# Optimization experiments

Hardware: AMD Instinct MI355X
Metric: run time of the kernel (lower is better)

## Reference

```python
import jax, jax.numpy as jnp
import numpy as np

B = 4096   # batch
V = 512    # num_variables
H = 64     # hidden_dim


def setup_inputs() -> dict:
    key = jax.random.key(0)
    ks = jax.random.split(key, 6)
    return {
        "X": jax.random.normal(ks[0], (B, V), dtype=jnp.float32),
        "adjacency_logits": jax.random.normal(ks[1], (V, V), dtype=jnp.float32) * 0.1,
        # W1[i] is the first Linear of net i: maps V inputs -> H hidden
        "W1": jax.random.normal(ks[2], (V, V, H), dtype=jnp.float32) * (1.0 / np.sqrt(V)),
        "b1": jax.random.normal(ks[3], (V, H), dtype=jnp.float32) * 0.01,
        # W2[i] is the second Linear of net i: maps H hidden -> 1 output
        "W2": jax.random.normal(ks[4], (V, H), dtype=jnp.float32) * (1.0 / np.sqrt(H)),
        "b2": jax.random.normal(ks[5], (V,), dtype=jnp.float32) * 0.01,
    }


def reference(X, adjacency_logits, W1, b1, W2, b2):
    # Hard adjacency (hard_adjacency=True path): threshold sigmoid, zero diagonal.
    probs = jax.nn.sigmoid(adjacency_logits)
    adj = (probs > 0.5).astype(X.dtype) * (1.0 - jnp.eye(V, dtype=X.dtype))  # [V, V]

    # Original loop: for each i, net_i(X * adj[:, i]).
    # Fold the parent mask into the first-layer weights: W1_eff[i, v, h] = W1[i, v, h] * adj[v, i]
    W1_eff = W1 * adj.T[:, :, None]                      # [V, V, H]
    h = jax.nn.relu(jnp.einsum('bv,ivh->bih', X, W1_eff) + b1[None])  # [B, V, H]
    reconstructed = jnp.einsum('bih,ih->bi', h, W2) + b2[None]        # [B, V]
    return reconstructed, adj
```

## Files before the change

kernel.cpp:

```cpp
#include <hip/hip_runtime.h>
#include <hip/hip_bf16.h>
#include <stdint.h>

#define BB 4096
#define VV 512
#define HH 64

typedef short bf16x8 __attribute__((ext_vector_type(8)));
typedef float floatx4 __attribute__((ext_vector_type(4)));
typedef unsigned short ushort8 __attribute__((ext_vector_type(8)));

typedef const __attribute__((address_space(1))) void g_void;
typedef __attribute__((address_space(3))) void l_void;

__device__ __forceinline__ void gload_lds16(const void* g, void* l) {
    __builtin_amdgcn_global_load_lds((g_void*)g, (l_void*)l, 16, 0, 0);
}

__device__ __forceinline__ unsigned short f2bf_rne(float f) {
    unsigned int u = __float_as_uint(f);
    u += 0x7FFFu + ((u >> 16) & 1u);
    return (unsigned short)(u >> 16);
}

__global__ __launch_bounds__(256) void adj_kernel(const float* __restrict__ logits,
                                                  float* __restrict__ adj_out) {
    int idx = blockIdx.x * 256 + threadIdx.x;
    int v = idx >> 9, u = idx & (VV - 1);
    adj_out[idx] = (logits[idx] > 0.0f && v != u) ? 1.0f : 0.0f;
}

__global__ __launch_bounds__(256) void prep_kernel(const float* __restrict__ X,
                                                   const float* __restrict__ logits,
                                                   float* __restrict__ adj_out,
                                                   unsigned short* __restrict__ Xp) {
    int idx = blockIdx.x * 256 + threadIdx.x;
    {
        int v = idx >> 9, u = idx & (VV - 1);
        adj_out[idx] = (logits[idx] > 0.0f && v != u) ? 1.0f : 0.0f;
    }
    {
        int lane = idx & 63;
        int mt   = (idx >> 6) & 3;
        int ks   = (idx >> 8) & 15;
        int rb   = idx >> 12;
        int row  = rb * 64 + mt * 16 + (lane & 15);
        int k0   = ks * 32 + (lane >> 4) * 8;
        const float* src = X + (size_t)row * VV + k0;
        ushort8 o;
        #pragma unroll
        for (int e = 0; e < 8; ++e) o[e] = f2bf_rne(src[e]);
        *(ushort8*)(Xp + (size_t)idx * 8) = o;
    }
}

__global__ __launch_bounds__(256) void w1_transform_kernel(const float* __restrict__ W1,
                                                           const float* __restrict__ logits,
                                                           unsigned short* __restrict__ W1t) {
    __shared__ float tile[64][65];
    __shared__ float maskv[64];
    int bx = blockIdx.x;
    int i  = bx >> 3;
    int v0 = (bx & 7) << 6;
    int t  = threadIdx.x;
    if (t < 64) {
        int v = v0 + t;
        maskv[t] = (logits[(size_t)v * VV + i] > 0.0f && v != i) ? 1.0f : 0.0f;
    }
    const float* src = W1 + ((size_t)i * VV + v0) * HH;
    #pragma unroll
    for (int j = 0; j < 16; ++j) {
        int idx = j * 256 + t;
        tile[idx >> 6][idx & 63] = src[idx];
    }
    __syncthreads();
    unsigned short* dst = W1t + (size_t)i * (HH * VV) + v0;
    #pragma unroll
    for (int j = 0; j < 2; ++j) {
        int c = j * 256 + t;
        int h = c >> 3;
        int vr0 = (c & 7) * 8;
        ushort8 o;
        #pragma unroll
        for (int r = 0; r < 8; ++r)
            o[r] = f2bf_rne(tile[vr0 + r][h] * maskv[vr0 + r]);
        *(ushort8*)&dst[(size_t)h * VV + vr0] = o;
    }
}

__global__ __launch_bounds__(256, 2) void dag_gemm_kernel(
        const unsigned short* __restrict__ Xp,
        const unsigned short* __restrict__ W1t,
        const float* __restrict__ b1,
        const float* __restrict__ W2,
        const float* __restrict__ b2,
        float* __restrict__ outT)
{
    __shared__ __align__(16) unsigned short Ws[HH * VV];
    __shared__ float Po[256];

    const int t    = threadIdx.x;
    const int wave = t >> 6;
    const int lane = t & 63;
    const int ln   = lane & 15;
    const int quad = lane >> 4;

    const int bx   = blockIdx.x;
    const int i    = bx >> 4;
    const int row0 = (bx & 15) << 8;

    const unsigned short* abase =
        Xp + (size_t)((row0 >> 6) + wave) * (64 * VV) + lane * 8;

    bf16x8 af[4][4];
    #pragma unroll
    for (int s = 0; s < 3; ++s)
        #pragma unroll
        for (int mt = 0; mt < 4; ++mt)
            af[s][mt] = *(const bf16x8*)(abase + (s * 4 + mt) * 512);

    const unsigned short* wbase = W1t + (size_t)i * (HH * VV);
    #pragma unroll
    for (int j = 0; j < 16; ++j) {
        int c = j * 256 + t;
        int h = c >> 6, s = c & 63;
        gload_lds16(wbase + (size_t)h * VV + (size_t)(s ^ (h & 7)) * 8,
                    (char*)Ws + c * 16);
    }
    __syncthreads();

    floatx4 acc[4][4];
    #pragma unroll
    for (int a = 0; a < 4; ++a)
        #pragma unroll
        for (int b = 0; b < 4; ++b)
            acc[a][b] = (floatx4){0.f, 0.f, 0.f, 0.f};

    bf16x8 bq[2][4];
    #pragma unroll
    for (int nt = 0; nt < 4; ++nt)
        bq[0][nt] = *(const bf16x8*)&Ws[(nt * 16 + ln) * VV + (quad ^ (ln & 7)) * 8];

    #pragma unroll
    for (int kk = 0; kk < 16; ++kk) {
        const int cur = kk & 1, nxt = cur ^ 1;
        if (kk < 13) {
            #pragma unroll
            for (int mt = 0; mt < 4; ++mt)
                af[(kk + 3) & 3][mt] =
                    *(const bf16x8*)(abase + ((kk + 3) * 4 + mt) * 512);
        }
        if (kk < 15) {
            #pragma unroll
            for (int nt = 0; nt < 4; ++nt)
                bq[nxt][nt] = *(const bf16x8*)
                    &Ws[(nt * 16 + ln) * VV + (((kk + 1) * 4 + quad) ^ (ln & 7)) * 8];
        }
        #pragma unroll
        for (int mt = 0; mt < 4; ++mt)
            #pragma unroll
            for (int nt = 0; nt < 4; ++nt)
                acc[mt][nt] = __builtin_amdgcn_mfma_f32_16x16x32_bf16(
                    af[kk & 3][mt], bq[cur][nt], acc[mt][nt], 0, 0, 0);
    }

    float b1v[4], w2v[4];
    #pragma unroll
    for (int nt = 0; nt < 4; ++nt) {
        b1v[nt] = b1[i * HH + nt * 16 + ln];
        w2v[nt] = W2[i * HH + nt * 16 + ln];
    }
    const float b2i = b2[i];
    #pragma unroll
    for (int mt = 0; mt < 4; ++mt) {
        #pragma unroll
        for (int r = 0; r < 4; ++r) {
            float p = 0.f;
            #pragma unroll
            for (int nt = 0; nt < 4; ++nt) {
                float hv = acc[mt][nt][r] + b1v[nt];
                hv = hv > 0.f ? hv : 0.f;
                p += hv * w2v[nt];
            }
            p += __shfl_xor(p, 8);
            p += __shfl_xor(p, 4);
            p += __shfl_xor(p, 2);
            p += __shfl_xor(p, 1);
            if (ln == 0)
                Po[wave * 64 + mt * 16 + quad * 4 + r] = p + b2i;
        }
    }
    __syncthreads();
    outT[(size_t)i * BB + row0 + wave * 64 + lane] = Po[wave * 64 + lane];
}

__global__ __launch_bounds__(256) void transpose_kernel(const float* __restrict__ outT,
                                                        float* __restrict__ out) {
    __shared__ float tile[64][65];
    int i0 = (blockIdx.x & 7) * 64;
    int r0 = (blockIdx.x >> 3) * 64;
    int t  = threadIdx.x;
    #pragma unroll
    for (int j = 0; j < 16; ++j) {
        int idx = j * 256 + t;
        int ii = idx >> 6, rr = idx & 63;
        tile[ii][rr] = outT[(size_t)(i0 + ii) * BB + r0 + rr];
    }
    __syncthreads();
    #pragma unroll
    for (int j = 0; j < 16; ++j) {
        int idx = j * 256 + t;
        int rr = idx >> 6, ii = idx & 63;
        out[(size_t)(r0 + rr) * VV + i0 + ii] = tile[ii][rr];
    }
}

__global__ __launch_bounds__(256) void fallback_kernel(
        const float* __restrict__ X, const float* __restrict__ logits,
        const float* __restrict__ W1, const float* __restrict__ b1,
        const float* __restrict__ W2, const float* __restrict__ b2,
        float* __restrict__ out) {
    __shared__ float Wc[128][64];
    int i   = blockIdx.x & (VV - 1);
    int row = (blockIdx.x >> 9) * 256 + threadIdx.x;
    float acc[64];
    #pragma unroll
    for (int h = 0; h < 64; ++h) acc[h] = 0.f;
    for (int v0 = 0; v0 < VV; v0 += 128) {
        __syncthreads();
        for (int j = 0; j < 32; ++j) {
            int idx = j * 256 + threadIdx.x;
            int vr = idx >> 6, h = idx & 63;
            int v = v0 + vr;
            float m = (logits[(size_t)v * VV + i] > 0.f && v != i) ? 1.f : 0.f;
            Wc[vr][h] = W1[((size_t)i * VV + v) * HH + h] * m;
        }
        __syncthreads();
        for (int vr = 0; vr < 128; ++vr) {
            float xv = X[(size_t)row * VV + v0 + vr];
            #pragma unroll
            for (int h = 0; h < 64; ++h) acc[h] += xv * Wc[vr][h];
        }
    }
    float p = b2[i];
    #pragma unroll
    for (int h = 0; h < 64; ++h) {
        float hv = acc[h] + b1[i * HH + h];
        p += (hv > 0.f ? hv : 0.f) * W2[i * HH + h];
    }
    out[(size_t)row * VV + i] = p;
}

extern "C" void kernel_launch(void* const* d_in, const int* in_sizes, int n_in,
                              void* d_out, int out_size, void* d_ws, size_t ws_size,
                              hipStream_t stream) {
    const float* X      = (const float*)d_in[0];
    const float* logits = (const float*)d_in[1];
    const float* W1     = (const float*)d_in[2];
    const float* b1     = (const float*)d_in[3];
    const float* W2     = (const float*)d_in[4];
    const float* b2     = (const float*)d_in[5];

    float* out     = (float*)d_out;
    float* adj_out = out + (size_t)BB * VV;

    const size_t xp_bytes   = (size_t)BB * VV * 2;
    const size_t w1t_bytes  = (size_t)VV * HH * VV * 2;
    const size_t outt_bytes = (size_t)BB * VV * 4;
    const size_t need = xp_bytes + w1t_bytes + outt_bytes;

    if (ws_size >= need) {
        unsigned short* Xp   = (unsigned short*)d_ws;
        unsigned short* W1t  = (unsigned short*)((char*)d_ws + xp_bytes);
        float*          outT = (float*)((char*)d_ws + xp_bytes + w1t_bytes);
        hipLaunchKernelGGL(prep_kernel, dim3((VV * VV) / 256), dim3(256), 0, stream,
                           X, logits, adj_out, Xp);
        hipLaunchKernelGGL(w1_transform_kernel, dim3(VV * (VV / 64)), dim3(256), 0, stream,
                           W1, logits, W1t);
        hipLaunchKernelGGL(dag_gemm_kernel, dim3(VV * (BB / 256)), dim3(256), 0, stream,
                           Xp, W1t, b1, W2, b2, outT);
        hipLaunchKernelGGL(transpose_kernel, dim3((BB / 64) * (VV / 64)), dim3(256), 0, stream,
                           outT, out);
    } else {
        hipLaunchKernelGGL(adj_kernel, dim3((VV * VV) / 256), dim3(256), 0, stream,
                           logits, adj_out);
        hipLaunchKernelGGL(fallback_kernel, dim3(VV * (BB / 256)), dim3(256), 0, stream,
                           X, logits, W1, b1, W2, b2, out);
    }
}
```

Before: 280.6 us.

## Make GEMM persistent with double-buffered W1 prefetch and fuse prep kernels

Merges the X-packing/adjacency kernel and the W1 transform into one launch. The GEMM becomes a persistent kernel of 256 blocks of 512 threads, each looping over 16 (variable, row-chunk) work items. The next item's W1 slice is prefetched into a second LDS buffer with async global-to-LDS loads, overlapped with the current item's MFMAs. This removes launch overhead and hides W1 load latency, but doubles LDS to 128KB per block, which limits occupancy to one block per CU. It also drops the 4096-block oversubscription, so load balance across CUs matters more.

```diff
diff --git a/kernel.cpp b/kernel.cpp
--- a/kernel.cpp
+++ b/kernel.cpp
@@ -30,65 +30,63 @@
     adj_out[idx] = (logits[idx] > 0.0f && v != u) ? 1.0f : 0.0f;
 }
 
-__global__ __launch_bounds__(256) void prep_kernel(const float* __restrict__ X,
-                                                   const float* __restrict__ logits,
-                                                   float* __restrict__ adj_out,
-                                                   unsigned short* __restrict__ Xp) {
-    int idx = blockIdx.x * 256 + threadIdx.x;
-    {
-        int v = idx >> 9, u = idx & (VV - 1);
-        adj_out[idx] = (logits[idx] > 0.0f && v != u) ? 1.0f : 0.0f;
-    }
-    {
-        int lane = idx & 63;
-        int mt   = (idx >> 6) & 3;
-        int ks   = (idx >> 8) & 15;
-        int rb   = idx >> 12;
-        int row  = rb * 64 + mt * 16 + (lane & 15);
-        int k0   = ks * 32 + (lane >> 4) * 8;
-        const float* src = X + (size_t)row * VV + k0;
-        ushort8 o;
-        #pragma unroll
-        for (int e = 0; e < 8; ++e) o[e] = f2bf_rne(src[e]);
-        *(ushort8*)(Xp + (size_t)idx * 8) = o;
-    }
-}
-
-__global__ __launch_bounds__(256) void w1_transform_kernel(const float* __restrict__ W1,
-                                                           const float* __restrict__ logits,
-                                                           unsigned short* __restrict__ W1t) {
+__global__ __launch_bounds__(256) void prep_fused_kernel(
+        const float* __restrict__ X, const float* __restrict__ logits,
+        const float* __restrict__ W1, float* __restrict__ adj_out,
+        unsigned short* __restrict__ Xp, unsigned short* __restrict__ W1t) {
     __shared__ float tile[64][65];
     __shared__ float maskv[64];
     int bx = blockIdx.x;
-    int i  = bx >> 3;
-    int v0 = (bx & 7) << 6;
     int t  = threadIdx.x;
-    if (t < 64) {
-        int v = v0 + t;
-        maskv[t] = (logits[(size_t)v * VV + i] > 0.0f && v != i) ? 1.0f : 0.0f;
-    }
-    const float* src = W1 + ((size_t)i * VV + v0) * HH;
-    #pragma unroll
-    for (int j = 0; j < 16; ++j) {
-        int idx = j * 256 + t;
-        tile[idx >> 6][idx & 63] = src[idx];
-    }
-    __syncthreads();
-    unsigned short* dst = W1t + (size_t)i * (HH * VV) + v0;
-    #pragma unroll
-    for (int j = 0; j < 2; ++j) {
-        int c = j * 256 + t;
-        int h = c >> 3;
-        int vr0 = (c & 7) * 8;
-        ushort8 o;
-        #pragma unroll
-        for (int r = 0; r < 8; ++r)
-            o[r] = f2bf_rne(tile[vr0 + r][h] * maskv[vr0 + r]);
-        *(ushort8*)&dst[(size_t)h * VV + vr0] = o;
-    }
-}
-
-__global__ __launch_bounds__(256, 2) void dag_gemm_kernel(
+    if (bx < 4096) {
+        int i  = bx >> 3;
+        int v0 = (bx & 7) << 6;
+        if (t < 64) {
+            int v = v0 + t;
+            maskv[t] = (logits[(size_t)v * VV + i] > 0.0f && v != i) ? 1.0f : 0.0f;
+        }
+        const float* src = W1 + ((size_t)i * VV + v0) * HH;
+        #pragma unroll
+        for (int j = 0; j < 16; ++j) {
+            int idx = j * 256 + t;
+            tile[idx >> 6][idx & 63] = src[idx];
+        }
+        __syncthreads();
+        unsigned short* dst = W1t + (size_t)i * (HH * VV) + v0;
+        #pragma unroll
+        for (int j = 0; j < 2; ++j) {
+            int c = j * 256 + t;
+            int h = c >> 3;
+            int vr0 = (c & 7) * 8;
+            ushort8 o;
+            #pragma unroll
+            for (int r = 0; r < 8; ++r)
+                o[r] = f2bf_rne(tile[vr0 + r][h] * maskv[vr0 + r]);
+            *(ushort8*)&dst[(size_t)h * VV + vr0] = o;
+        }
+    } else {
+        int idx = (bx - 4096) * 256 + t;
+        {
+            int v = idx >> 9, u = idx & (VV - 1);
+            adj_out[idx] = (logits[idx] > 0.0f && v != u) ? 1.0f : 0.0f;
+        }
+        {
+            int lane = idx & 63;
+            int mt   = (idx >> 6) & 3;
+            int ks   = (idx >> 8) & 15;
+            int rb   = idx >> 12;
+            int row  = rb * 64 + mt * 16 + (lane & 15);
+            int k0   = ks * 32 + (lane >> 4) * 8;
+            const float* src = X + (size_t)row * VV + k0;
+            ushort8 o;
+            #pragma unroll
+            for (int e = 0; e < 8; ++e) o[e] = f2bf_rne(src[e]);
+            *(ushort8*)(Xp + (size_t)idx * 8) = o;
+        }
+    }
+}
+
+__global__ __launch_bounds__(512, 2) void dag_gemm_kernel(
         const unsigned short* __restrict__ Xp,
         const unsigned short* __restrict__ W1t,
         const float* __restrict__ b1,
@@ -96,8 +94,8 @@
         const float* __restrict__ b2,
         float* __restrict__ outT)
 {
-    __shared__ __align__(16) unsigned short Ws[HH * VV];
-    __shared__ float Po[256];
+    __shared__ __align__(16) unsigned short Ws[2][HH * VV];
+    __shared__ float Po[512];
 
     const int t    = threadIdx.x;
     const int wave = t >> 6;
@@ -105,93 +103,117 @@
     const int ln   = lane & 15;
     const int quad = lane >> 4;
 
-    const int bx   = blockIdx.x;
-    const int i    = bx >> 4;
-    const int row0 = (bx & 15) << 8;
-
-    const unsigned short* abase =
-        Xp + (size_t)((row0 >> 6) + wave) * (64 * VV) + lane * 8;
-
-    bf16x8 af[4][4];
-    #pragma unroll
-    for (int s = 0; s < 3; ++s)
-        #pragma unroll
-        for (int mt = 0; mt < 4; ++mt)
-            af[s][mt] = *(const bf16x8*)(abase + (s * 4 + mt) * 512);
-
-    const unsigned short* wbase = W1t + (size_t)i * (HH * VV);
-    #pragma unroll
-    for (int j = 0; j < 16; ++j) {
-        int c = j * 256 + t;
-        int h = c >> 6, s = c & 63;
-        gload_lds16(wbase + (size_t)h * VV + (size_t)(s ^ (h & 7)) * 8,
-                    (char*)Ws + c * 16);
+    const int x = blockIdx.x & 7;
+    const int j = blockIdx.x >> 3;
+
+    {
+        int i0 = x * 64 + (j >> 3);
+        const unsigned short* wbase = W1t + (size_t)i0 * (HH * VV);
+        #pragma unroll
+        for (int c8 = 0; c8 < 8; ++c8) {
+            int c = c8 * 512 + t;
+            int h = c >> 6, s = c & 63;
+            gload_lds16(wbase + (size_t)h * VV + (size_t)(s ^ (h & 7)) * 8,
+                        (char*)Ws[0] + c * 16);
+        }
     }
     __syncthreads();
 
-    floatx4 acc[4][4];
-    #pragma unroll
-    for (int a = 0; a < 4; ++a)
-        #pragma unroll
-        for (int b = 0; b < 4; ++b)
-            acc[a][b] = (floatx4){0.f, 0.f, 0.f, 0.f};
-
-    bf16x8 bq[2][4];
-    #pragma unroll
-    for (int nt = 0; nt < 4; ++nt)
-        bq[0][nt] = *(const bf16x8*)&Ws[(nt * 16 + ln) * VV + (quad ^ (ln & 7)) * 8];
-
-    #pragma unroll
-    for (int kk = 0; kk < 16; ++kk) {
-        const int cur = kk & 1, nxt = cur ^ 1;
-        if (kk < 13) {
+    #pragma unroll 1
+    for (int n = 0; n < 16; ++n) {
+        const int g     = n * 32 + j;
+        const int i     = x * 64 + (g >> 3);
+        const int chunk = g & 7;
+        const int buf   = n & 1;
+
+        const unsigned short* wnext = W1t;
+        if (n < 15) {
+            int gn = (n + 1) * 32 + j;
+            wnext = W1t + (size_t)(x * 64 + (gn >> 3)) * (HH * VV);
+        }
+
+        const unsigned short* abase =
+            Xp + (size_t)(chunk * 8 + wave) * (64 * VV) + lane * 8;
+
+        bf16x8 af[4][4];
+        #pragma unroll
+        for (int s = 0; s < 3; ++s)
             #pragma unroll
             for (int mt = 0; mt < 4; ++mt)
-                af[(kk + 3) & 3][mt] =
-                    *(const bf16x8*)(abase + ((kk + 3) * 4 + mt) * 512);
-        }
-        if (kk < 15) {
-            #pragma unroll
-            for (int nt = 0; nt < 4; ++nt)
-                bq[nxt][nt] = *(const bf16x8*)
-                    &Ws[(nt * 16 + ln) * VV + (((kk + 1) * 4 + quad) ^ (ln & 7)) * 8];
-        }
-        #pragma unroll
-        for (int mt = 0; mt < 4; ++mt)
-            #pragma unroll
-            for (int nt = 0; nt < 4; ++nt)
-                acc[mt][nt] = __builtin_amdgcn_mfma_f32_16x16x32_bf16(
-                    af[kk & 3][mt], bq[cur][nt], acc[mt][nt], 0, 0, 0);
-    }
-
-    float b1v[4], w2v[4];
-    #pragma unroll
-    for (int nt = 0; nt < 4; ++nt) {
-        b1v[nt] = b1[i * HH + nt * 16 + ln];
-        w2v[nt] = W2[i * HH + nt * 16 + ln];
-    }
-    const float b2i = b2[i];
-    #pragma unroll
-    for (int mt = 0; mt < 4; ++mt) {
-        #pragma unroll
-        for (int r = 0; r < 4; ++r) {
-            float p = 0.f;
-            #pragma unroll
-            for (int nt = 0; nt < 4; ++nt) {
-                float hv = acc[mt][nt][r] + b1v[nt];
-                hv = hv > 0.f ? hv : 0.f;
-                p += hv * w2v[nt];
+                af[s][mt] = *(const bf16x8*)(abase + (s * 4 + mt) * 512);
+
+        floatx4 acc[4][4];
+        #pragma unroll
+        for (int a = 0; a < 4; ++a)
+            #pragma unroll
+            for (int b = 0; b < 4; ++b)
+                acc[a][b] = (floatx4){0.f, 0.f, 0.f, 0.f};
+
+        const unsigned short* wsb = Ws[buf];
+        bf16x8 bq[2][4];
+        #pragma unroll
+        for (int nt = 0; nt < 4; ++nt)
+            bq[0][nt] = *(const bf16x8*)
+                &wsb[(nt * 16 + ln) * VV + (quad ^ (ln & 7)) * 8];
+
+        #pragma unroll
+        for (int kk = 0; kk < 16; ++kk) {
+            if (kk < 8 && n < 15) {
+                int c = kk * 512 + t;
+                int h = c >> 6, s = c & 63;
+                gload_lds16(wnext + (size_t)h * VV + (size_t)(s ^ (h & 7)) * 8,
+                            (char*)Ws[buf ^ 1] + c * 16);
             }
-            p += __shfl_xor(p, 8);
-            p += __shfl_xor(p, 4);
-            p += __shfl_xor(p, 2);
-            p += __shfl_xor(p, 1);
-            if (ln == 0)
-                Po[wave * 64 + mt * 16 + quad * 4 + r] = p + b2i;
-        }
-    }
-    __syncthreads();
-    outT[(size_t)i * BB + row0 + wave * 64 + lane] = Po[wave * 64 + lane];
+            if (kk < 13) {
+                #pragma unroll
+                for (int mt = 0; mt < 4; ++mt)
+                    af[(kk + 3) & 3][mt] =
+                        *(const bf16x8*)(abase + ((kk + 3) * 4 + mt) * 512);
+            }
+            if (kk < 15) {
+                #pragma unroll
+                for (int nt = 0; nt < 4; ++nt)
+                    bq[(kk + 1) & 1][nt] = *(const bf16x8*)
+                        &wsb[(nt * 16 + ln) * VV +
+                             (((kk + 1) * 4 + quad) ^ (ln & 7)) * 8];
+            }
+            #pragma unroll
+            for (int mt = 0; mt < 4; ++mt)
+                #pragma unroll
+                for (int nt = 0; nt < 4; ++nt)
+                    acc[mt][nt] = __builtin_amdgcn_mfma_f32_16x16x32_bf16(
+                        af[kk & 3][mt], bq[kk & 1][nt], acc[mt][nt], 0, 0, 0);
+        }
+
+        float b1v[4], w2v[4];
+        #pragma unroll
+        for (int nt = 0; nt < 4; ++nt) {
+            b1v[nt] = b1[i * HH + nt * 16 + ln];
+            w2v[nt] = W2[i * HH + nt * 16 + ln];
+        }
+        const float b2i = b2[i];
+        #pragma unroll
+        for (int mt = 0; mt < 4; ++mt) {
+            #pragma unroll
+            for (int r = 0; r < 4; ++r) {
+                float p = 0.f;
+                #pragma unroll
+                for (int nt = 0; nt < 4; ++nt) {
+                    float hv = acc[mt][nt][r] + b1v[nt];
+                    hv = hv > 0.f ? hv : 0.f;
+                    p += hv * w2v[nt];
+                }
+                p += __shfl_xor(p, 8);
+                p += __shfl_xor(p, 4);
+                p += __shfl_xor(p, 2);
+                p += __shfl_xor(p, 1);
+                if (ln == 0)
+                    Po[wave * 64 + mt * 16 + quad * 4 + r] = p + b2i;
+            }
+        }
+        outT[(size_t)i * BB + chunk * 512 + t] = Po[t];
+        __syncthreads();
+    }
 }
 
 __global__ __launch_bounds__(256) void transpose_kernel(const float* __restrict__ outT,
@@ -273,11 +295,9 @@
         unsigned short* Xp   = (unsigned short*)d_ws;
         unsigned short* W1t  = (unsigned short*)((char*)d_ws + xp_bytes);
         float*          outT = (float*)((char*)d_ws + xp_bytes + w1t_bytes);
-        hipLaunchKernelGGL(prep_kernel, dim3((VV * VV) / 256), dim3(256), 0, stream,
-                           X, logits, adj_out, Xp);
-        hipLaunchKernelGGL(w1_transform_kernel, dim3(VV * (VV / 64)), dim3(256), 0, stream,
-                           W1, logits, W1t);
-        hipLaunchKernelGGL(dag_gemm_kernel, dim3(VV * (BB / 256)), dim3(256), 0, stream,
+        hipLaunchKernelGGL(prep_fused_kernel, dim3(5120), dim3(256), 0, stream,
+                           X, logits, W1, adj_out, Xp, W1t);
+        hipLaunchKernelGGL(dag_gemm_kernel, dim3(256), dim3(512), 0, stream,
                            Xp, W1t, b1, W2, b2, outT);
         hipLaunchKernelGGL(transpose_kernel, dim3((BB / 64) * (VV / 64)), dim3(256), 0, stream,
                            outT, out);
```

After: 517.4 us. 84.4% more time.

## Reuse LDS weight tile across four row passes and fuse prep kernels

Applied to the files above, without the earlier changes.

Each GEMM block now loads one net's masked bf16 W1 slice into LDS once and reuses it over four passes of 256 batch rows. This cuts the grid from 8192 to 2048 blocks and quarters the repeated weight loads from global memory. Blocks are mapped so the four blocks sharing a net land on the same XCD. Separately, the X conversion, adjacency and W1 transform kernels are merged into one launch, saving a launch gap. The trade-off is fewer blocks, which may reduce latency hiding, and passes within a block are serialized.

```diff
diff --git a/kernel.cpp b/kernel.cpp
--- a/kernel.cpp
+++ b/kernel.cpp
@@ -30,61 +30,59 @@
     adj_out[idx] = (logits[idx] > 0.0f && v != u) ? 1.0f : 0.0f;
 }
 
-__global__ __launch_bounds__(256) void prep_kernel(const float* __restrict__ X,
-                                                   const float* __restrict__ logits,
-                                                   float* __restrict__ adj_out,
-                                                   unsigned short* __restrict__ Xp) {
-    int idx = blockIdx.x * 256 + threadIdx.x;
-    {
-        int v = idx >> 9, u = idx & (VV - 1);
-        adj_out[idx] = (logits[idx] > 0.0f && v != u) ? 1.0f : 0.0f;
-    }
-    {
-        int lane = idx & 63;
-        int mt   = (idx >> 6) & 3;
-        int ks   = (idx >> 8) & 15;
-        int rb   = idx >> 12;
-        int row  = rb * 64 + mt * 16 + (lane & 15);
-        int k0   = ks * 32 + (lane >> 4) * 8;
-        const float* src = X + (size_t)row * VV + k0;
-        ushort8 o;
-        #pragma unroll
-        for (int e = 0; e < 8; ++e) o[e] = f2bf_rne(src[e]);
-        *(ushort8*)(Xp + (size_t)idx * 8) = o;
-    }
-}
-
-__global__ __launch_bounds__(256) void w1_transform_kernel(const float* __restrict__ W1,
-                                                           const float* __restrict__ logits,
-                                                           unsigned short* __restrict__ W1t) {
+__global__ __launch_bounds__(256) void prep_fused_kernel(
+        const float* __restrict__ X, const float* __restrict__ logits,
+        const float* __restrict__ W1, float* __restrict__ adj_out,
+        unsigned short* __restrict__ Xp, unsigned short* __restrict__ W1t) {
     __shared__ float tile[64][65];
     __shared__ float maskv[64];
     int bx = blockIdx.x;
-    int i  = bx >> 3;
-    int v0 = (bx & 7) << 6;
     int t  = threadIdx.x;
-    if (t < 64) {
-        int v = v0 + t;
-        maskv[t] = (logits[(size_t)v * VV + i] > 0.0f && v != i) ? 1.0f : 0.0f;
-    }
-    const float* src = W1 + ((size_t)i * VV + v0) * HH;
-    #pragma unroll
-    for (int j = 0; j < 16; ++j) {
-        int idx = j * 256 + t;
-        tile[idx >> 6][idx & 63] = src[idx];
-    }
-    __syncthreads();
-    unsigned short* dst = W1t + (size_t)i * (HH * VV) + v0;
-    #pragma unroll
-    for (int j = 0; j < 2; ++j) {
-        int c = j * 256 + t;
-        int h = c >> 3;
-        int vr0 = (c & 7) * 8;
-        ushort8 o;
-        #pragma unroll
-        for (int r = 0; r < 8; ++r)
-            o[r] = f2bf_rne(tile[vr0 + r][h] * maskv[vr0 + r]);
-        *(ushort8*)&dst[(size_t)h * VV + vr0] = o;
+    if (bx < 4096) {
+        int i  = bx >> 3;
+        int v0 = (bx & 7) << 6;
+        if (t < 64) {
+            int v = v0 + t;
+            maskv[t] = (logits[(size_t)v * VV + i] > 0.0f && v != i) ? 1.0f : 0.0f;
+        }
+        const float* src = W1 + ((size_t)i * VV + v0) * HH;
+        #pragma unroll
+        for (int j = 0; j < 16; ++j) {
+            int idx = j * 256 + t;
+            tile[idx >> 6][idx & 63] = src[idx];
+        }
+        __syncthreads();
+        unsigned short* dst = W1t + (size_t)i * (HH * VV) + v0;
+        #pragma unroll
+        for (int j = 0; j < 2; ++j) {
+            int c = j * 256 + t;
+            int h = c >> 3;
+            int vr0 = (c & 7) * 8;
+            ushort8 o;
+            #pragma unroll
+            for (int r = 0; r < 8; ++r)
+                o[r] = f2bf_rne(tile[vr0 + r][h] * maskv[vr0 + r]);
+            *(ushort8*)&dst[(size_t)h * VV + vr0] = o;
+        }
+    } else {
+        int idx = (bx - 4096) * 256 + t;
+        {
+            int v = idx >> 9, u = idx & (VV - 1);
+            adj_out[idx] = (logits[idx] > 0.0f && v != u) ? 1.0f : 0.0f;
+        }
+        {
+            int lane = idx & 63;
+            int mt   = (idx >> 6) & 3;
+            int ks   = (idx >> 8) & 15;
+            int rb   = idx >> 12;
+            int row  = rb * 64 + mt * 16 + (lane & 15);
+            int k0   = ks * 32 + (lane >> 4) * 8;
+            const float* src = X + (size_t)row * VV + k0;
+            ushort8 o;
+            #pragma unroll
+            for (int e = 0; e < 8; ++e) o[e] = f2bf_rne(src[e]);
+            *(ushort8*)(Xp + (size_t)idx * 8) = o;
+        }
     }
 }
 
@@ -105,19 +103,11 @@
     const int ln   = lane & 15;
     const int quad = lane >> 4;
 
-    const int bx   = blockIdx.x;
-    const int i    = bx >> 4;
-    const int row0 = (bx & 15) << 8;
-
-    const unsigned short* abase =
-        Xp + (size_t)((row0 >> 6) + wave) * (64 * VV) + lane * 8;
-
-    bf16x8 af[4][4];
-    #pragma unroll
-    for (int s = 0; s < 3; ++s)
-        #pragma unroll
-        for (int mt = 0; mt < 4; ++mt)
-            af[s][mt] = *(const bf16x8*)(abase + (s * 4 + mt) * 512);
+    const int bx = blockIdx.x;
+    const int x  = bx & 7;
+    const int r  = bx >> 3;
+    const int i  = x * 64 + (r >> 2);
+    const int c4 = r & 3;
 
     const unsigned short* wbase = W1t + (size_t)i * (HH * VV);
     #pragma unroll
@@ -127,42 +117,6 @@
         gload_lds16(wbase + (size_t)h * VV + (size_t)(s ^ (h & 7)) * 8,
                     (char*)Ws + c * 16);
     }
-    __syncthreads();
-
-    floatx4 acc[4][4];
-    #pragma unroll
-    for (int a = 0; a < 4; ++a)
-        #pragma unroll
-        for (int b = 0; b < 4; ++b)
-            acc[a][b] = (floatx4){0.f, 0.f, 0.f, 0.f};
-
-    bf16x8 bq[2][4];
-    #pragma unroll
-    for (int nt = 0; nt < 4; ++nt)
-        bq[0][nt] = *(const bf16x8*)&Ws[(nt * 16 + ln) * VV + (quad ^ (ln & 7)) * 8];
-
-    #pragma unroll
-    for (int kk = 0; kk < 16; ++kk) {
-        const int cur = kk & 1, nxt = cur ^ 1;
-        if (kk < 13) {
-            #pragma unroll
-            for (int mt = 0; mt < 4; ++mt)
-                af[(kk + 3) & 3][mt] =
-                    *(const bf16x8*)(abase + ((kk + 3) * 4 + mt) * 512);
-        }
-        if (kk < 15) {
-            #pragma unroll
-            for (int nt = 0; nt < 4; ++nt)
-                bq[nxt][nt] = *(const bf16x8*)
-                    &Ws[(nt * 16 + ln) * VV + (((kk + 1) * 4 + quad) ^ (ln & 7)) * 8];
-        }
-        #pragma unroll
-        for (int mt = 0; mt < 4; ++mt)
-            #pragma unroll
-            for (int nt = 0; nt < 4; ++nt)
-                acc[mt][nt] = __builtin_amdgcn_mfma_f32_16x16x32_bf16(
-                    af[kk & 3][mt], bq[cur][nt], acc[mt][nt], 0, 0, 0);
-    }
 
     float b1v[4], w2v[4];
     #pragma unroll
@@ -171,27 +125,79 @@
         w2v[nt] = W2[i * HH + nt * 16 + ln];
     }
     const float b2i = b2[i];
-    #pragma unroll
-    for (int mt = 0; mt < 4; ++mt) {
-        #pragma unroll
-        for (int r = 0; r < 4; ++r) {
-            float p = 0.f;
-            #pragma unroll
-            for (int nt = 0; nt < 4; ++nt) {
-                float hv = acc[mt][nt][r] + b1v[nt];
-                hv = hv > 0.f ? hv : 0.f;
-                p += hv * w2v[nt];
+
+    __syncthreads();
+
+    #pragma unroll 1
+    for (int pass = 0; pass < 4; ++pass) {
+        const int rb0 = c4 * 16 + pass * 4;
+        const unsigned short* abase =
+            Xp + (size_t)(rb0 + wave) * (64 * VV) + lane * 8;
+
+        bf16x8 af[4][4];
+        #pragma unroll
+        for (int s = 0; s < 3; ++s)
+            #pragma unroll
+            for (int mt = 0; mt < 4; ++mt)
+                af[s][mt] = *(const bf16x8*)(abase + (s * 4 + mt) * 512);
+
+        floatx4 acc[4][4];
+        #pragma unroll
+        for (int a = 0; a < 4; ++a)
+            #pragma unroll
+            for (int b = 0; b < 4; ++b)
+                acc[a][b] = (floatx4){0.f, 0.f, 0.f, 0.f};
+
+        bf16x8 bq[2][4];
+        #pragma unroll
+        for (int nt = 0; nt < 4; ++nt)
+            bq[0][nt] = *(const bf16x8*)
+                &Ws[(nt * 16 + ln) * VV + (quad ^ (ln & 7)) * 8];
+
+        #pragma unroll
+        for (int kk = 0; kk < 16; ++kk) {
+            if (kk < 13) {
+                #pragma unroll
+                for (int mt = 0; mt < 4; ++mt)
+                    af[(kk + 3) & 3][mt] =
+                        *(const bf16x8*)(abase + ((kk + 3) * 4 + mt) * 512);
             }
-            p += __shfl_xor(p, 8);
-            p += __shfl_xor(p, 4);
-            p += __shfl_xor(p, 2);
-            p += __shfl_xor(p, 1);
-            if (ln == 0)
-                Po[wave * 64 + mt * 16 + quad * 4 + r] = p + b2i;
-        }
-    }
-    __syncthreads();
-    outT[(size_t)i * BB + row0 + wave * 64 + lane] = Po[wave * 64 + lane];
+            if (kk < 15) {
+                #pragma unroll
+                for (int nt = 0; nt < 4; ++nt)
+                    bq[(kk + 1) & 1][nt] = *(const bf16x8*)
+                        &Ws[(nt * 16 + ln) * VV +
+                            (((kk + 1) * 4 + quad) ^ (ln & 7)) * 8];
+            }
+            #pragma unroll
+            for (int mt = 0; mt < 4; ++mt)
+                #pragma unroll
+                for (int nt = 0; nt < 4; ++nt)
+                    acc[mt][nt] = __builtin_amdgcn_mfma_f32_16x16x32_bf16(
+                        af[kk & 3][mt], bq[kk & 1][nt], acc[mt][nt], 0, 0, 0);
+        }
+
+        #pragma unroll
+        for (int mt = 0; mt < 4; ++mt) {
+            #pragma unroll
+            for (int rr = 0; rr < 4; ++rr) {
+                float p = 0.f;
+                #pragma unroll
+                for (int nt = 0; nt < 4; ++nt) {
+                    float hv = acc[mt][nt][rr] + b1v[nt];
+                    hv = hv > 0.f ? hv : 0.f;
+                    p += hv * w2v[nt];
+                }
+                p += __shfl_xor(p, 8);
+                p += __shfl_xor(p, 4);
+                p += __shfl_xor(p, 2);
+                p += __shfl_xor(p, 1);
+                if (ln == 0)
+                    Po[wave * 64 + mt * 16 + quad * 4 + rr] = p + b2i;
+            }
+        }
+        outT[(size_t)i * BB + rb0 * 64 + wave * 64 + lane] = Po[wave * 64 + lane];
+    }
 }
 
 __global__ __launch_bounds__(256) void transpose_kernel(const float* __restrict__ outT,
@@ -273,11 +279,9 @@
         unsigned short* Xp   = (unsigned short*)d_ws;
         unsigned short* W1t  = (unsigned short*)((char*)d_ws + xp_bytes);
         float*          outT = (float*)((char*)d_ws + xp_bytes + w1t_bytes);
-        hipLaunchKernelGGL(prep_kernel, dim3((VV * VV) / 256), dim3(256), 0, stream,
-                           X, logits, adj_out, Xp);
-        hipLaunchKernelGGL(w1_transform_kernel, dim3(VV * (VV / 64)), dim3(256), 0, stream,
-                           W1, logits, W1t);
-        hipLaunchKernelGGL(dag_gemm_kernel, dim3(VV * (BB / 256)), dim3(256), 0, stream,
+        hipLaunchKernelGGL(prep_fused_kernel, dim3(5120), dim3(256), 0, stream,
+                           X, logits, W1, adj_out, Xp, W1t);
+        hipLaunchKernelGGL(dag_gemm_kernel, dim3(2048), dim3(256), 0, stream,
                            Xp, W1t, b1, W2, b2, outT);
         hipLaunchKernelGGL(transpose_kernel, dim3((BB / 64) * (VV / 64)), dim3(256), 0, stream,
                            outT, out);
```

New measurement: 516.4 us. +84.0%, slower.
